# Kernel optimization log

Hardware: AMD Instinct MI355X
Metric: run time of the kernel (lower is better)

Reference implementation:

```python
import jax, jax.numpy as jnp
import numpy as np
from jax import lax

N, C_IN, HID, HP = 32, 512, 512, 28     # instances, channels, hidden, pooled res
NPATCH, HS = 25, 112                    # part channels (24+1), heatmap size
K_DYN, ATT_HID = 3, 64                  # dynamic-conv banks, attention hidden
BN_EPS = 1e-5


def setup_inputs() -> dict:
    key = jax.random.key(0)
    ks = jax.random.split(key, 20)
    g = lambda k, s, sc: sc * jax.random.normal(k, s, jnp.float32)

    features = g(ks[0], (N, C_IN, HP, HP), 1.0)
    # structured fine_segm so argmax class pattern covers all classes per row/col
    hh = jnp.arange(HS)[:, None]
    ww = jnp.arange(HS)[None, :]
    cls = (hh + ww) % NPATCH                                    # [H,W]
    base = 5.0 * jnp.transpose(jax.nn.one_hot(cls, NPATCH, dtype=jnp.float32), (2, 0, 1))
    fine_segm = base[None] + g(ks[1], (N, NPATCH, HS, HS), 0.5)
    u = jax.random.uniform(ks[2], (N, NPATCH, HS, HS), jnp.float32)
    v = jax.random.uniform(ks[3], (N, NPATCH, HS, HS), jnp.float32)

    return dict(
        features=features, fine_segm=fine_segm, u=u, v=v,
        conv1_w=g(ks[4], (HID, C_IN, 3, 3), 0.02), conv1_b=jnp.zeros((HID,), jnp.float32),
        conv2_w=g(ks[5], (HID, HID, 3, 3), 0.02), conv2_b=jnp.zeros((HID,), jnp.float32),
        att1_fc1_w=g(ks[6], (ATT_HID, 5), 0.1), att1_fc1_b=jnp.zeros((ATT_HID,), jnp.float32),
        att1_fc2_w=g(ks[7], (K_DYN, ATT_HID), 0.1), att1_fc2_b=jnp.zeros((K_DYN,), jnp.float32),
        dyn1_w=g(ks[8], (K_DYN, HID, HID, 3, 3), 0.02),
        att2_fc1_w=g(ks[9], (ATT_HID, 1), 0.1), att2_fc1_b=jnp.zeros((ATT_HID,), jnp.float32),
        att2_fc2_w=g(ks[10], (K_DYN, ATT_HID), 0.1), att2_fc2_b=jnp.zeros((K_DYN,), jnp.float32),
        dyn2_w=g(ks[11], (K_DYN, HID, HID, 3, 3), 0.02),
        bn1_g=1.0 + g(ks[12], (HID,), 0.1), bn1_b=g(ks[13], (HID,), 0.05),
        bn1_m=g(ks[14], (HID,), 0.1), bn1_v=jax.random.uniform(ks[15], (HID,), jnp.float32, 0.5, 1.5),
        bn2_g=1.0 + g(ks[16], (HID,), 0.1), bn2_b=g(ks[17], (HID,), 0.05),
        bn2_m=g(ks[18], (HID,), 0.1), bn2_v=jax.random.uniform(ks[19], (HID,), jnp.float32, 0.5, 1.5),
    )


def _conv2d(x, w, b=None):
    y = lax.conv_general_dilated(x, w, (1, 1), 'SAME',
                                 dimension_numbers=('NCHW', 'OIHW', 'NCHW'))
    return y if b is None else y + b[None, :, None, None]


def _bn(x, g, b, m, vv):
    inv = g / jnp.sqrt(vv + BN_EPS)
    return (x - m[None, :, None, None]) * inv[None, :, None, None] + b[None, :, None, None]


def _dyn_conv(stat, x, fc1_w, fc1_b, fc2_w, fc2_b, W):
    # attention over K kernel banks from globally pooled stats
    pooled = stat.mean(axis=(2, 3))                              # [B, Cin_att]
    h = jax.nn.relu(pooled @ fc1_w.T + fc1_b)                    # [B, ATT_HID]
    att = jax.nn.softmax(h @ fc2_w.T + fc2_b, axis=1)            # [B, K]
    Wb = jnp.einsum('bk,koihw->boihw', att, W)                   # per-sample kernels
    conv1 = lambda xi, wi: _conv2d(xi[None], wi)[0]
    return jax.vmap(conv1)(x, Wb)


def _local_linear(i, u, v):
    c = i.shape[1]
    mask = jnp.transpose(jax.nn.one_hot(jnp.argmax(i, axis=1), c, dtype=i.dtype), (0, 3, 1, 2))
    ue = (u * mask)[:, 1:]
    ve = (v * mask)[:, 1:]
    m = mask[:, 1:]
    u_mean = ue.sum(3, keepdims=True) / m.sum(3, keepdims=True)   # per-row mean
    v_mean = ve.sum(2, keepdims=True) / m.sum(2, keepdims=True)   # per-col mean
    u_var = jnp.sqrt((((ue - u_mean) ** 2) * m).sum(3) / m.sum(3))  # [B,C-1,H]
    v_var = jnp.sqrt((((ve - v_mean) ** 2) * m).sum(2) / m.sum(2))  # [B,C-1,W]
    var = jnp.sqrt(jnp.einsum('bch,bcw->bchw', u_var, v_var))
    return lax.stop_gradient(jnp.exp(-var.sum(1, keepdims=True)))   # [B,1,H,W]


def reference(features, fine_segm, u, v,
              conv1_w, conv1_b, conv2_w, conv2_b,
              att1_fc1_w, att1_fc1_b, att1_fc2_w, att1_fc2_b, dyn1_w,
              att2_fc1_w, att2_fc1_b, att2_fc2_w, att2_fc2_b, dyn2_w,
              bn1_g, bn1_b, bn1_m, bn1_v, bn2_g, bn2_b, bn2_m, bn2_v):
    x = jax.nn.relu(_conv2d(features, conv1_w, conv1_b))
    x = jax.nn.relu(_conv2d(x, conv2_w, conv2_b))
    identity = x

    p = jax.nn.softmax(fine_segm, axis=1)
    tv, _ = lax.top_k(jnp.moveaxis(p, 1, -1), 4)                 # [B,H,W,4]
    tv = jnp.moveaxis(tv, -1, 1)                                 # [B,4,H,W]
    stat1 = jnp.concatenate([tv, tv.mean(axis=1, keepdims=True)], axis=1)  # [B,5,H,W]
    stat2 = _local_linear(fine_segm, u, v)                       # [B,1,H,W]

    out = _dyn_conv(stat1, x, att1_fc1_w, att1_fc1_b, att1_fc2_w, att1_fc2_b, dyn1_w)
    out = jax.nn.relu(_bn(out, bn1_g, bn1_b, bn1_m, bn1_v))
    out = _dyn_conv(stat2, out, att2_fc1_w, att2_fc1_b, att2_fc2_w, att2_fc2_b, dyn2_w)
    out = _bn(out, bn2_g, bn2_b, bn2_m, bn2_v)
    return jax.nn.relu(out + identity)
```

## Files before the change

### kernel.cpp

```cpp
#include <hip/hip_runtime.h>
#include <math.h>

#define NB 32
#define CIN 512
#define HIDC 512
#define HP 28
#define PIX 784
#define NPCH 25
#define HS 112
#define HS2 12544
#define ATTH 64
#define BN_EPS 1e-5f

typedef unsigned short ushortT;
typedef __attribute__((ext_vector_type(8))) short s16x8;
typedef __attribute__((ext_vector_type(4))) float f32x4;

__device__ __forceinline__ float bf2f(unsigned bits16) {
    union { unsigned u; float f; } c; c.u = bits16 << 16; return c.f;
}
__device__ __forceinline__ unsigned f2bf_rne(float f) {
    union { float f; unsigned u; } c; c.f = f;
    unsigned u = c.u;
    u += 0x7FFFu + ((u >> 16) & 1u);
    return u >> 16;
}
__device__ __forceinline__ float asf_u(unsigned v) {
    union { unsigned u; float f; } c; c.u = v; return c.f;
}
__device__ __forceinline__ unsigned blendpair(unsigned u0, unsigned u1, unsigned u2,
                                              float a0, float a1, float a2) {
    float lo = a0*asf_u(u0 << 16) + a1*asf_u(u1 << 16) + a2*asf_u(u2 << 16);
    float hi = a0*asf_u(u0 & 0xFFFF0000u) + a1*asf_u(u1 & 0xFFFF0000u) + a2*asf_u(u2 & 0xFFFF0000u);
    union { float f; unsigned u; } cl, chh; cl.f = lo; chh.f = hi;
    return (cl.u >> 16) | (chh.u & 0xFFFF0000u);
}
__device__ __forceinline__ uint4 blend4(uint4 v0, uint4 v1, uint4 v2,
                                        float a0, float a1, float a2) {
    uint4 r;
    r.x = blendpair(v0.x, v1.x, v2.x, a0, a1, a2);
    r.y = blendpair(v0.y, v1.y, v2.y, a0, a1, a2);
    r.z = blendpair(v0.z, v1.z, v2.z, a0, a1, a2);
    r.w = blendpair(v0.w, v1.w, v2.w, a0, a1, a2);
    return r;
}

__global__ __launch_bounds__(256)
void nchw2nhwc_bf16(const float* __restrict__ in, ushortT* __restrict__ out)
{
    __shared__ float tile[64][65];
    const int b  = blockIdx.z;
    const int c0 = blockIdx.y * 64;
    const int p0 = blockIdx.x * 64;
    const int tid = threadIdx.x;
    for (int i = tid; i < 4096; i += 256) {
        int cc = i >> 6, pp = i & 63;
        float v = 0.f;
        if (p0 + pp < PIX) v = in[((size_t)b*CIN + c0 + cc)*PIX + p0 + pp];
        tile[cc][pp] = v;
    }
    __syncthreads();
    for (int i = tid; i < 4096; i += 256) {
        int pp = i >> 6, cc = i & 63;
        if (p0 + pp < PIX)
            out[((size_t)b*PIX + p0 + pp)*CIN + c0 + cc] = (ushortT)f2bf_rne(tile[cc][pp]);
    }
}

__global__ __launch_bounds__(256)
void wtrans_kernel(const float* __restrict__ w, ushortT* __restrict__ wt)
{
    __shared__ float buf[4608];
    const int oc = blockIdx.x, bank = blockIdx.y;
    const float* src = w + (size_t)bank*HIDC*CIN*9 + (size_t)oc*CIN*9;
    for (int i = threadIdx.x; i < 4608; i += 256) buf[i] = src[i];
    __syncthreads();
    for (int i = threadIdx.x; i < 4608; i += 256) {
        int t = i / 512, ic = i - t*512;
        wt[(((size_t)bank*9 + t)*HIDC + oc)*CIN + ic] = (ushortT)f2bf_rne(buf[(size_t)ic*9 + t]);
    }
}

template<int MODE>
__global__ __launch_bounds__(256, 2)
void conv_mfma(const ushortT* __restrict__ xin,
               const ushortT* __restrict__ wt,
               const float* __restrict__ bias,
               const float* __restrict__ scale,
               const float* __restrict__ shift,
               const float* __restrict__ att,
               const ushortT* __restrict__ addsrc,
               ushortT* __restrict__ outb,
               float* __restrict__ outf)
{
    __shared__ __align__(16) ushortT xs[480*64];
    __shared__ __align__(16) ushortT wsA[2][4096];

    const int tid  = threadIdx.x;
    const int lane = tid & 63;
    const int ph   = tid >> 6;
    const int lrow = lane & 15;
    const int lgrp = lane >> 4;

    const int oc0 = blockIdx.x * 64;
    const int sh  = blockIdx.y;
    const int b   = blockIdx.z;

    float a0 = 0.f, a1 = 0.f, a2 = 0.f;
    if (MODE != 0) { a0 = att[b*3+0]; a1 = att[b*3+1]; a2 = att[b*3+2]; }

    int pq[7];
#pragma unroll
    for (int nf = 0; nf < 7; ++nf) {
        int q = ph*98 + nf*16 + lrow;
        int qc = q < 392 ? q : 391;
        int r = qc / 28;
        pq[nf] = r*30 + (qc - r*28);
    }

    int afoff[2][4];
#pragma unroll
    for (int kk = 0; kk < 2; ++kk)
#pragma unroll
        for (int mf = 0; mf < 4; ++mf) {
            int ocl = mf*16 + lrow;
            afoff[kk][mf] = (ocl*8 + ((kk*4+lgrp) ^ (ocl&7)))*8;
        }

    int woff[2], wdst[2];
#pragma unroll
    for (int i = 0; i < 2; ++i) {
        int j = tid + i*256;
        int ocl = j >> 3, o = j & 7;
        woff[i] = ocl*CIN + o*8;
        wdst[i] = (ocl*8 + (o ^ (ocl&7)))*8;
    }

    f32x4 acc[4][7];
#pragma unroll
    for (int mf = 0; mf < 4; ++mf)
#pragma unroll
        for (int nf = 0; nf < 7; ++nf) acc[mf][nf] = (f32x4)0.f;

    const ushortT* xb = xin + (size_t)b * PIX * CIN;
    const size_t BANKS = (size_t)9*HIDC*CIN;

    auto stage_x = [&](int ic0) {
#pragma unroll
        for (int i = 0; i < 15; ++i) {
            int j = tid + i*256;
            int p = j >> 3, o = j & 7;
            int row = p / 30, col = p - row*30;
            int gh = sh*14 + row - 1, gw = col - 1;
            uint4 val = make_uint4(0u,0u,0u,0u);
            if ((unsigned)gh < 28u && (unsigned)gw < 28u)
                val = *(const uint4*)(xb + ((size_t)(gh*28 + gw)*CIN + ic0 + o*8));
            *(uint4*)(xs + (size_t)((p*8 + (o ^ (p&7)))*8)) = val;
        }
    };

    stage_x(0);
    {
        const ushortT* wA = wt + (size_t)oc0*CIN;
#pragma unroll
        for (int i = 0; i < 2; ++i) {
            uint4 v0 = *(const uint4*)(wA + woff[i]);
            uint4 val = v0;
            if (MODE != 0) {
                uint4 v1 = *(const uint4*)(wA + woff[i] + BANKS);
                uint4 v2 = *(const uint4*)(wA + woff[i] + 2*BANKS);
                val = blend4(v0, v1, v2, a0, a1, a2);
            }
            *(uint4*)(&wsA[0][0] + wdst[i]) = val;
        }
    }
    __syncthreads();

    uint4 p0[2], p1[2], p2[2];
    for (int k = 0; k < 72; ++k) {
        const int ch  = k / 9;
        const int t   = k - ch*9;
        const int cur = k & 1;
        const bool pf = (k < 71);
        const int kn  = k + 1;
        const int chn = kn / 9, tn = kn - chn*9;

        if (pf) {
            const ushortT* wA = wt + ((size_t)tn*HIDC + oc0)*CIN + chn*64;
#pragma unroll
            for (int i = 0; i < 2; ++i) {
                p0[i] = *(const uint4*)(wA + woff[i]);
                if (MODE != 0) {
                    p1[i] = *(const uint4*)(wA + woff[i] + BANKS);
                    p2[i] = *(const uint4*)(wA + woff[i] + 2*BANKS);
                }
            }
        }

        const int dh = (t >= 6) ? 2 : (t >= 3 ? 1 : 0);
        const int dw = t - dh*3;
        const int doff = dh*30 + dw;
        const ushortT* wbuf = &wsA[cur][0];
#pragma unroll
        for (int kk = 0; kk < 2; ++kk) {
            const int ob = kk*4 + lgrp;
            s16x8 af[4];
#pragma unroll
            for (int mf = 0; mf < 4; ++mf)
                af[mf] = *(const s16x8*)(wbuf + afoff[kk][mf]);
#pragma unroll
            for (int nf = 0; nf < 7; ++nf) {
                int pp = pq[nf] + doff;
                s16x8 bv = *(const s16x8*)(xs + (size_t)((pp*8 + (ob ^ (pp&7)))*8));
#pragma unroll
                for (int mf = 0; mf < 4; ++mf)
                    acc[mf][nf] = __builtin_amdgcn_mfma_f32_16x16x32_bf16(af[mf], bv, acc[mf][nf], 0, 0, 0);
            }
        }

        if (pf) {
            ushortT* wb = &wsA[cur^1][0];
#pragma unroll
            for (int i = 0; i < 2; ++i) {
                uint4 val;
                if (MODE == 0) val = p0[i];
                else           val = blend4(p0[i], p1[i], p2[i], a0, a1, a2);
                *(uint4*)(wb + wdst[i]) = val;
            }
            if (t == 8) {
                __syncthreads();
                stage_x(chn*64);
            }
        }
        __syncthreads();
    }

    const int q0 = ph * 98;
#pragma unroll
    for (int mf = 0; mf < 4; ++mf) {
        const int oc = oc0 + mf*16 + lgrp*4;
        float sc[4], shv[4];
#pragma unroll
        for (int jj = 0; jj < 4; ++jj) {
            if (MODE == 0) { sc[jj] = 1.f; shv[jj] = bias[oc+jj]; }
            else           { sc[jj] = scale[oc+jj]; shv[jj] = shift[oc+jj]; }
        }
#pragma unroll
        for (int nf = 0; nf < 7; ++nf) {
            const int qrel = nf*16 + lrow;
            if (qrel < 98) {
                const int p = sh*392 + q0 + qrel;
                f32x4 a = acc[mf][nf];
                if (MODE == 2) {
                    const ushortT* id = addsrc + ((size_t)b*PIX + p)*CIN + oc;
                    ushort4 iv = *(const ushort4*)id;
                    float v0 = fmaxf(a.x*sc[0] + shv[0] + bf2f(iv.x), 0.f);
                    float v1 = fmaxf(a.y*sc[1] + shv[1] + bf2f(iv.y), 0.f);
                    float v2 = fmaxf(a.z*sc[2] + shv[2] + bf2f(iv.z), 0.f);
                    float v3 = fmaxf(a.w*sc[3] + shv[3] + bf2f(iv.w), 0.f);
                    float* op = outf + ((size_t)b*HIDC + oc)*PIX + p;
                    op[0*PIX] = v0; op[1*PIX] = v1; op[2*PIX] = v2; op[3*PIX] = v3;
                } else {
                    float v0 = fmaxf(a.x*sc[0] + shv[0], 0.f);
                    float v1 = fmaxf(a.y*sc[1] + shv[1], 0.f);
                    float v2 = fmaxf(a.z*sc[2] + shv[2], 0.f);
                    float v3 = fmaxf(a.w*sc[3] + shv[3], 0.f);
                    ushort4 o4;
                    o4.x = (ushortT)f2bf_rne(v0); o4.y = (ushortT)f2bf_rne(v1);
                    o4.z = (ushortT)f2bf_rne(v2); o4.w = (ushortT)f2bf_rne(v3);
                    *(ushort4*)(outb + ((size_t)b*PIX + p)*CIN + oc) = o4;
                }
            }
        }
    }
}

template<int MODE>
__global__ __launch_bounds__(256)
void conv3x3_kernel(const float* __restrict__ x,
                    const float* __restrict__ w,
                    const float* __restrict__ bias,
                    const float* __restrict__ att,
                    const float* __restrict__ bnscale,
                    const float* __restrict__ bnshift,
                    const float* __restrict__ addsrc,
                    float* __restrict__ out)
{
    const int tid = threadIdx.x;
    const int o0  = blockIdx.x * 8;
    const int b   = blockIdx.y;
    __shared__ float xsb[30*30];
    __shared__ float wsm[72];
    float a0 = 0.f, a1 = 0.f, a2 = 0.f;
    if (MODE != 0) { a0 = att[b*3+0]; a1 = att[b*3+1]; a2 = att[b*3+2]; }
    float acc[8][4];
#pragma unroll
    for (int o = 0; o < 8; ++o)
#pragma unroll
        for (int s = 0; s < 4; ++s) acc[o][s] = 0.f;
    const float* xbp = x + (size_t)b * CIN * PIX;
    for (int i = 0; i < CIN; ++i) {
        const float* xc = xbp + (size_t)i * PIX;
        for (int idx = tid; idx < 900; idx += 256) {
            int r = idx / 30, c = idx - r*30;
            float v = 0.f;
            if (r >= 1 && r <= HP && c >= 1 && c <= HP) v = xc[(r-1)*HP + (c-1)];
            xsb[idx] = v;
        }
        if (tid < 72) {
            int o = tid / 9, tap = tid - o*9;
            float wv;
            if (MODE == 0) wv = w[((size_t)(o0+o)*CIN + i)*9 + tap];
            else {
                size_t base = ((size_t)(o0+o)*CIN + i)*9 + tap;
                size_t bank = (size_t)HIDC*CIN*9;
                wv = a0*w[base] + a1*w[base+bank] + a2*w[base+2*bank];
            }
            wsm[tid] = wv;
        }
        __syncthreads();
        float xwin[4][9];
#pragma unroll
        for (int s = 0; s < 4; ++s) {
            int p = tid + s*256; if (p > PIX-1) p = PIX-1;
            int h = p / HP, wc = p - h*HP;
#pragma unroll
            for (int t = 0; t < 9; ++t) {
                int dh = t/3, dw = t - dh*3;
                xwin[s][t] = xsb[(h+dh)*30 + (wc+dw)];
            }
        }
#pragma unroll
        for (int o = 0; o < 8; ++o) {
            float wr[9];
#pragma unroll
            for (int t = 0; t < 9; ++t) wr[t] = wsm[o*9+t];
#pragma unroll
            for (int s = 0; s < 4; ++s) {
                float sum = acc[o][s];
#pragma unroll
                for (int t = 0; t < 9; ++t) sum = fmaf(wr[t], xwin[s][t], sum);
                acc[o][s] = sum;
            }
        }
        __syncthreads();
    }
#pragma unroll
    for (int s = 0; s < 4; ++s) {
        int p = tid + s*256;
        if (p >= PIX) continue;
#pragma unroll
        for (int o = 0; o < 8; ++o) {
            int oc = o0 + o;
            float v = acc[o][s];
            if (MODE == 0) v += bias[oc];
            else           v = v * bnscale[oc] + bnshift[oc];
            if (MODE == 2) v += addsrc[((size_t)b*HIDC + oc)*PIX + p];
            v = fmaxf(v, 0.f);
            out[((size_t)b*HIDC + oc)*PIX + p] = v;
        }
    }
}

__global__ __launch_bounds__(256)
void stat1_kernel(const float* __restrict__ fs, float* __restrict__ part)
{
    const int b = blockIdx.y, chunk = blockIdx.x, tid = threadIdx.x;
    const float* f = fs + (size_t)b * NPCH * HS2;
    const int lo = chunk * 14 * HS, hi = lo + 14 * HS;
    float s0=0.f, s1=0.f, s2=0.f, s3=0.f;
    for (int pos = lo + tid; pos < hi; pos += 256) {
        float t0=-1e30f, t1=-1e30f, t2=-1e30f, t3=-1e30f;
        for (int c = 0; c < NPCH; ++c) {
            float v = f[(size_t)c*HS2 + pos];
            if      (v > t0) { t3=t2; t2=t1; t1=t0; t0=v; }
            else if (v > t1) { t3=t2; t2=t1; t1=v; }
            else if (v > t2) { t3=t2; t2=v; }
            else if (v > t3) { t3=v; }
        }
        float denom = 0.f;
        for (int c = 0; c < NPCH; ++c) denom += expf(f[(size_t)c*HS2 + pos] - t0);
        float inv = 1.f / denom;
        s0 += inv;
        s1 += expf(t1 - t0) * inv;
        s2 += expf(t2 - t0) * inv;
        s3 += expf(t3 - t0) * inv;
    }
    __shared__ float red[256];
    float vals[4] = {s0, s1, s2, s3};
    for (int j = 0; j < 4; ++j) {
        red[tid] = vals[j];
        __syncthreads();
        for (int off = 128; off; off >>= 1) {
            if (tid < off) red[tid] += red[tid + off];
            __syncthreads();
        }
        if (tid == 0) part[((size_t)b*8 + chunk)*4 + j] = red[0];
        __syncthreads();
    }
}

__global__ void cls_kernel(const float* __restrict__ fs, int* __restrict__ cls)
{
    int idx = blockIdx.x*256 + threadIdx.x;
    if (idx >= NB*HS2) return;
    int b = idx / HS2, pos = idx - b*HS2;
    const float* f = fs + (size_t)b*NPCH*HS2 + pos;
    float best = f[0]; int bi = 0;
    for (int c = 1; c < NPCH; ++c) {
        float v = f[(size_t)c*HS2];
        if (v > best) { best = v; bi = c; }
    }
    cls[idx] = bi;
}

__global__ __launch_bounds__(256)
void rowstat_kernel(const float* __restrict__ u, const int* __restrict__ cls,
                    float* __restrict__ uvar)
{
    int wid = blockIdx.x*4 + (threadIdx.x >> 6);
    int lane = threadIdx.x & 63;
    int h = wid % HS, t = wid / HS, c = t % 24, b = t / 24;
    const int*   cr = cls + (size_t)b*HS2 + (size_t)h*HS;
    const float* ur = u + (((size_t)b*NPCH + c + 1)*HS + h)*HS;
    float cnt = 0.f, s = 0.f, s2 = 0.f;
    for (int wc = lane; wc < HS; wc += 64) {
        if (cr[wc] == c + 1) { float v = ur[wc]; cnt += 1.f; s += v; s2 += v*v; }
    }
    for (int off = 32; off; off >>= 1) {
        cnt += __shfl_down(cnt, off);
        s   += __shfl_down(s, off);
        s2  += __shfl_down(s2, off);
    }
    if (lane == 0) {
        float mean = s / cnt;
        uvar[wid] = sqrtf(fmaxf(s2/cnt - mean*mean, 0.f));
    }
}

__global__ void colstat_kernel(const float* __restrict__ v, const int* __restrict__ cls,
                               float* __restrict__ vvar)
{
    int idx = blockIdx.x*256 + threadIdx.x;
    if (idx >= NB*24*HS) return;
    int wc = idx % HS, t = idx / HS, c = t % 24, b = t / 24;
    const int*   cbase = cls + (size_t)b*HS2 + wc;
    const float* vbase = v + (((size_t)b*NPCH + c + 1)*HS)*HS + wc;
    float cnt = 0.f, s = 0.f, s2 = 0.f;
    for (int h = 0; h < HS; ++h) {
        if (cbase[(size_t)h*HS] == c + 1) {
            float val = vbase[(size_t)h*HS];
            cnt += 1.f; s += val; s2 += val*val;
        }
    }
    float mean = s / cnt;
    vvar[idx] = sqrtf(fmaxf(s2/cnt - mean*mean, 0.f));
}

__global__ __launch_bounds__(256)
void stat2_kernel(const float* __restrict__ uvar, const float* __restrict__ vvar,
                  float* __restrict__ pooled2p)
{
    const int b = blockIdx.x, seg = blockIdx.y, tid = threadIdx.x;
    __shared__ float us[24*HS], vs[24*HS], red[256];
    for (int i = tid; i < 24*HS; i += 256) {
        us[i] = uvar[(size_t)b*24*HS + i];
        vs[i] = vvar[(size_t)b*24*HS + i];
    }
    __syncthreads();
    float local = 0.f;
    const int lo = seg*1568, hi = lo + 1568;
    for (int pos = lo + tid; pos < hi; pos += 256) {
        int h = pos / HS, wc = pos - h*HS;
        float sum = 0.f;
        for (int c = 0; c < 24; ++c) sum += sqrtf(us[c*HS+h] * vs[c*HS+wc]);
        local += expf(-sum);
    }
    red[tid] = local;
    __syncthreads();
    for (int off = 128; off; off >>= 1) {
        if (tid < off) red[tid] += red[tid + off];
        __syncthreads();
    }
    if (tid == 0) pooled2p[b*8 + seg] = red[0];
}

__global__ __launch_bounds__(256)
void mlp_kernel(const float* __restrict__ part, const float* __restrict__ pooled2p,
                const float* __restrict__ a1w1, const float* __restrict__ a1b1,
                const float* __restrict__ a1w2, const float* __restrict__ a1b2,
                const float* __restrict__ a2w1, const float* __restrict__ a2b1,
                const float* __restrict__ a2w2, const float* __restrict__ a2b2,
                const float* __restrict__ bn1g, const float* __restrict__ bn1b,
                const float* __restrict__ bn1m, const float* __restrict__ bn1v,
                const float* __restrict__ bn2g, const float* __restrict__ bn2b,
                const float* __restrict__ bn2m, const float* __restrict__ bn2v,
                float* __restrict__ att1, float* __restrict__ att2,
                float* __restrict__ bnsc)
{
    const int tid = threadIdx.x;
    if (tid < NB) {
        int b = tid;
        float p[5]; float tot = 0.f;
        for (int j = 0; j < 4; ++j) {
            float s = 0.f;
            for (int ch = 0; ch < 8; ++ch) s += part[((size_t)b*8 + ch)*4 + j];
            p[j] = s / (float)HS2; tot += p[j];
        }
        p[4] = tot * 0.25f;
        float lg[3] = {a1b2[0], a1b2[1], a1b2[2]};
        for (int j = 0; j < ATTH; ++j) {
            float hv = a1b1[j];
            for (int t = 0; t < 5; ++t) hv += a1w1[j*5+t] * p[t];
            hv = fmaxf(hv, 0.f);
            for (int k = 0; k < 3; ++k) lg[k] += a1w2[k*ATTH+j] * hv;
        }
        float mx = fmaxf(fmaxf(lg[0], lg[1]), lg[2]);
        float e0 = expf(lg[0]-mx), e1 = expf(lg[1]-mx), e2 = expf(lg[2]-mx);
        float inv = 1.f / (e0+e1+e2);
        att1[b*3+0] = e0*inv; att1[b*3+1] = e1*inv; att1[b*3+2] = e2*inv;
    } else if (tid < 2*NB) {
        int b = tid - NB;
        float psum = 0.f;
        for (int j = 0; j < 8; ++j) psum += pooled2p[b*8 + j];
        float p = psum / (float)HS2;
        float lg[3] = {a2b2[0], a2b2[1], a2b2[2]};
        for (int j = 0; j < ATTH; ++j) {
            float hv = fmaxf(a2b1[j] + a2w1[j] * p, 0.f);
            for (int k = 0; k < 3; ++k) lg[k] += a2w2[k*ATTH+j] * hv;
        }
        float mx = fmaxf(fmaxf(lg[0], lg[1]), lg[2]);
        float e0 = expf(lg[0]-mx), e1 = expf(lg[1]-mx), e2 = expf(lg[2]-mx);
        float inv = 1.f / (e0+e1+e2);
        att2[b*3+0] = e0*inv; att2[b*3+1] = e1*inv; att2[b*3+2] = e2*inv;
    }
    for (int o = tid; o < HIDC; o += 256) {
        float sc1 = bn1g[o] / sqrtf(bn1v[o] + BN_EPS);
        bnsc[o]          = sc1;
        bnsc[512 + o]    = bn1b[o] - bn1m[o]*sc1;
        float sc2 = bn2g[o] / sqrtf(bn2v[o] + BN_EPS);
        bnsc[1024 + o]   = sc2;
        bnsc[1536 + o]   = bn2b[o] - bn2m[o]*sc2;
    }
}

extern "C" void kernel_launch(void* const* d_in, const int* in_sizes, int n_in,
                              void* d_out, int out_size, void* d_ws, size_t ws_size,
                              hipStream_t stream)
{
    (void)in_sizes; (void)n_in; (void)out_size;
    const float* features = (const float*)d_in[0];
    const float* fine_segm= (const float*)d_in[1];
    const float* u        = (const float*)d_in[2];
    const float* v        = (const float*)d_in[3];
    const float* conv1_w  = (const float*)d_in[4];
    const float* conv1_b  = (const float*)d_in[5];
    const float* conv2_w  = (const float*)d_in[6];
    const float* conv2_b  = (const float*)d_in[7];
    const float* a1w1     = (const float*)d_in[8];
    const float* a1b1     = (const float*)d_in[9];
    const float* a1w2     = (const float*)d_in[10];
    const float* a1b2     = (const float*)d_in[11];
    const float* dyn1_w   = (const float*)d_in[12];
    const float* a2w1     = (const float*)d_in[13];
    const float* a2b1     = (const float*)d_in[14];
    const float* a2w2     = (const float*)d_in[15];
    const float* a2b2     = (const float*)d_in[16];
    const float* dyn2_w   = (const float*)d_in[17];
    const float* bn1g     = (const float*)d_in[18];
    const float* bn1b     = (const float*)d_in[19];
    const float* bn1m     = (const float*)d_in[20];
    const float* bn1v     = (const float*)d_in[21];
    const float* bn2g     = (const float*)d_in[22];
    const float* bn2b     = (const float*)d_in[23];
    const float* bn2m     = (const float*)d_in[24];
    const float* bn2v     = (const float*)d_in[25];

    const size_t XB_BYTES = (size_t)NB*PIX*CIN*2;
    const size_t WT_BYTES = (size_t)3*9*HIDC*CIN*2;
    const size_t NEED = XB_BYTES*2 + WT_BYTES + 2308096;

    if (ws_size >= NEED) {
        char* wsb = (char*)d_ws;
        ushortT* xbuf = (ushortT*)wsb;
        ushortT* x2   = (ushortT*)(wsb + XB_BYTES);
        ushortT* wt   = (ushortT*)(wsb + 2*XB_BYTES);
        float* sm     = (float*)(wsb + 2*XB_BYTES + WT_BYTES);
        float* part    = sm;  sm += 1024;
        float* pooled2 = sm;  sm += 256;
        float* att1    = sm;  sm += 96;
        float* att2    = sm;  sm += 96;
        float* bnsc    = sm;  sm += 2048;
        float* uvar    = sm;  sm += NB*24*HS;
        float* vvar    = sm;  sm += NB*24*HS;
        int*   cls     = (int*)sm;
        ushortT* x1    = (ushortT*)d_out;

        nchw2nhwc_bf16<<<dim3(13, 8, NB), 256, 0, stream>>>(features, xbuf);
        wtrans_kernel<<<dim3(512, 1), 256, 0, stream>>>(conv1_w, wt);
        conv_mfma<0><<<dim3(8, 2, NB), 256, 0, stream>>>(
            xbuf, wt, conv1_b, nullptr, nullptr, nullptr, nullptr, x1, nullptr);
        wtrans_kernel<<<dim3(512, 1), 256, 0, stream>>>(conv2_w, wt);
        conv_mfma<0><<<dim3(8, 2, NB), 256, 0, stream>>>(
            x1, wt, conv2_b, nullptr, nullptr, nullptr, nullptr, x2, nullptr);

        stat1_kernel<<<dim3(8, NB), 256, 0, stream>>>(fine_segm, part);
        cls_kernel<<<(NB*HS2 + 255)/256, 256, 0, stream>>>(fine_segm, cls);
        rowstat_kernel<<<(NB*24*HS)/4, 256, 0, stream>>>(u, cls, uvar);
        colstat_kernel<<<(NB*24*HS + 255)/256, 256, 0, stream>>>(v, cls, vvar);
        stat2_kernel<<<dim3(NB, 8), 256, 0, stream>>>(uvar, vvar, pooled2);
        mlp_kernel<<<1, 256, 0, stream>>>(part, pooled2,
            a1w1, a1b1, a1w2, a1b2, a2w1, a2b1, a2w2, a2b2,
            bn1g, bn1b, bn1m, bn1v, bn2g, bn2b, bn2m, bn2v,
            att1, att2, bnsc);

        wtrans_kernel<<<dim3(512, 3), 256, 0, stream>>>(dyn1_w, wt);
        conv_mfma<1><<<dim3(8, 2, NB), 256, 0, stream>>>(
            x2, wt, nullptr, bnsc, bnsc + 512, att1, nullptr, xbuf, nullptr);
        wtrans_kernel<<<dim3(512, 3), 256, 0, stream>>>(dyn2_w, wt);
        conv_mfma<2><<<dim3(8, 2, NB), 256, 0, stream>>>(
            xbuf, wt, nullptr, bnsc + 1024, bnsc + 1536, att2, x2, nullptr, (float*)d_out);
    } else {
        const size_t BIG = (size_t)NB * HIDC * PIX;
        float* x1y1 = (float*)d_out;
        float* ws0  = (float*)d_ws;
        float* sm   = ws0 + BIG;
        float* part    = sm;  sm += 1024;
        float* pooled2 = sm;  sm += 256;
        float* att1    = sm;  sm += 96;
        float* att2    = sm;  sm += 96;
        float* bnsc    = sm;  sm += 2048;
        float* uvar    = sm;  sm += NB*24*HS;
        float* vvar    = sm;  sm += NB*24*HS;
        int*   cls     = (int*)sm;

        conv3x3_kernel<0><<<dim3(64, NB), 256, 0, stream>>>(
            features, conv1_w, conv1_b, nullptr, nullptr, nullptr, nullptr, x1y1);
        conv3x3_kernel<0><<<dim3(64, NB), 256, 0, stream>>>(
            x1y1, conv2_w, conv2_b, nullptr, nullptr, nullptr, nullptr, ws0);
        stat1_kernel<<<dim3(8, NB), 256, 0, stream>>>(fine_segm, part);
        cls_kernel<<<(NB*HS2 + 255)/256, 256, 0, stream>>>(fine_segm, cls);
        rowstat_kernel<<<(NB*24*HS)/4, 256, 0, stream>>>(u, cls, uvar);
        colstat_kernel<<<(NB*24*HS + 255)/256, 256, 0, stream>>>(v, cls, vvar);
        stat2_kernel<<<dim3(NB, 8), 256, 0, stream>>>(uvar, vvar, pooled2);
        mlp_kernel<<<1, 256, 0, stream>>>(part, pooled2,
            a1w1, a1b1, a1w2, a1b2, a2w1, a2b1, a2w2, a2b2,
            bn1g, bn1b, bn1m, bn1v, bn2g, bn2b, bn2m, bn2v,
            att1, att2, bnsc);
        conv3x3_kernel<1><<<dim3(64, NB), 256, 0, stream>>>(
            ws0, dyn1_w, nullptr, att1, bnsc, bnsc + 512, nullptr, x1y1);
        conv3x3_kernel<2><<<dim3(64, NB), 256, 0, stream>>>(
            x1y1, dyn2_w, nullptr, att2, bnsc + 1024, bnsc + 1536, ws0, ws0);
        hipMemcpyAsync(d_out, ws0, BIG * sizeof(float), hipMemcpyDeviceToDevice, stream);
    }
}
```

Before: 825.5 us.

## Software-pipeline LDS B-fragment loads in conv MFMA loop and fuse argmax into stat1

Restructures the conv MFMA inner loop into channel-chunk by tap loops with double-buffered register B fragments (PB/QB). Next tap's B loads are issued while the current half's MFMAs run, and MFMA blocks are wrapped in s_setprio. The intent is to hide LDS read latency behind matrix work, at the cost of more VGPR use. Separately, the argmax class computation is folded into the stat1 top-4 kernel, removing one kernel launch and a second full read of fine_segm.

```diff
diff --git a/kernel.cpp b/kernel.cpp
--- a/kernel.cpp
+++ b/kernel.cpp
@@ -158,6 +158,9 @@
             *(uint4*)(xs + (size_t)((p*8 + (o ^ (p&7)))*8)) = val;
         }
     };
+    auto baddr = [&](int pp) {
+        return (pp*8 + (lgrp ^ (pp&7)))*16;
+    };
 
     stage_x(0);
     {
@@ -176,63 +179,88 @@
     }
     __syncthreads();
 
+    s16x8 PB[7], QB[7];
     uint4 p0[2], p1[2], p2[2];
-    for (int k = 0; k < 72; ++k) {
-        const int ch  = k / 9;
-        const int t   = k - ch*9;
-        const int cur = k & 1;
-        const bool pf = (k < 71);
-        const int kn  = k + 1;
-        const int chn = kn / 9, tn = kn - chn*9;
-
-        if (pf) {
-            const ushortT* wA = wt + ((size_t)tn*HIDC + oc0)*CIN + chn*64;
-#pragma unroll
-            for (int i = 0; i < 2; ++i) {
-                p0[i] = *(const uint4*)(wA + woff[i]);
-                if (MODE != 0) {
-                    p1[i] = *(const uint4*)(wA + woff[i] + BANKS);
-                    p2[i] = *(const uint4*)(wA + woff[i] + 2*BANKS);
+
+    for (int c = 0; c < 8; ++c) {
+#pragma unroll
+        for (int nf = 0; nf < 7; ++nf)
+            PB[nf] = *(const s16x8*)((const char*)xs + baddr(pq[nf]));
+
+#pragma unroll
+        for (int t = 0; t < 9; ++t) {
+            const int k   = c*9 + t;
+            const int cur = k & 1;
+            const bool pf = (k < 71);
+            const int tn  = (t == 8) ? 0 : (t + 1);
+            const int chn = (t == 8) ? (c + 1) : c;
+            const ushortT* wbuf = &wsA[cur][0];
+
+            if (pf) {
+                const ushortT* wA = wt + ((size_t)tn*HIDC + oc0)*CIN + chn*64;
+#pragma unroll
+                for (int i = 0; i < 2; ++i) {
+                    p0[i] = *(const uint4*)(wA + woff[i]);
+                    if (MODE != 0) {
+                        p1[i] = *(const uint4*)(wA + woff[i] + BANKS);
+                        p2[i] = *(const uint4*)(wA + woff[i] + 2*BANKS);
+                    }
                 }
             }
-        }
-
-        const int dh = (t >= 6) ? 2 : (t >= 3 ? 1 : 0);
-        const int dw = t - dh*3;
-        const int doff = dh*30 + dw;
-        const ushortT* wbuf = &wsA[cur][0];
-#pragma unroll
-        for (int kk = 0; kk < 2; ++kk) {
-            const int ob = kk*4 + lgrp;
-            s16x8 af[4];
+
+            const int doff  = (t/3)*30 + (t%3);
+            const int doffn = ((t+1)/3)*30 + ((t+1)%3);
+
+            s16x8 af0[4];
 #pragma unroll
             for (int mf = 0; mf < 4; ++mf)
-                af[mf] = *(const s16x8*)(wbuf + afoff[kk][mf]);
-#pragma unroll
-            for (int nf = 0; nf < 7; ++nf) {
-                int pp = pq[nf] + doff;
-                s16x8 bv = *(const s16x8*)(xs + (size_t)((pp*8 + (ob ^ (pp&7)))*8));
+                af0[mf] = *(const s16x8*)(wbuf + afoff[0][mf]);
+#pragma unroll
+            for (int nf = 0; nf < 7; ++nf)
+                QB[nf] = *(const s16x8*)((const char*)xs + (baddr(pq[nf]+doff) ^ 64));
+
+            __builtin_amdgcn_s_setprio(1);
+#pragma unroll
+            for (int nf = 0; nf < 7; ++nf)
 #pragma unroll
                 for (int mf = 0; mf < 4; ++mf)
-                    acc[mf][nf] = __builtin_amdgcn_mfma_f32_16x16x32_bf16(af[mf], bv, acc[mf][nf], 0, 0, 0);
-            }
-        }
-
-        if (pf) {
-            ushortT* wb = &wsA[cur^1][0];
-#pragma unroll
-            for (int i = 0; i < 2; ++i) {
-                uint4 val;
-                if (MODE == 0) val = p0[i];
-                else           val = blend4(p0[i], p1[i], p2[i], a0, a1, a2);
-                *(uint4*)(wb + wdst[i]) = val;
-            }
-            if (t == 8) {
-                __syncthreads();
-                stage_x(chn*64);
-            }
-        }
-        __syncthreads();
+                    acc[mf][nf] = __builtin_amdgcn_mfma_f32_16x16x32_bf16(af0[mf], PB[nf], acc[mf][nf], 0, 0, 0);
+            __builtin_amdgcn_s_setprio(0);
+
+            s16x8 af1[4];
+#pragma unroll
+            for (int mf = 0; mf < 4; ++mf)
+                af1[mf] = *(const s16x8*)(wbuf + afoff[1][mf]);
+            if (t < 8) {
+#pragma unroll
+                for (int nf = 0; nf < 7; ++nf)
+                    PB[nf] = *(const s16x8*)((const char*)xs + baddr(pq[nf]+doffn));
+            }
+
+            __builtin_amdgcn_s_setprio(1);
+#pragma unroll
+            for (int nf = 0; nf < 7; ++nf)
+#pragma unroll
+                for (int mf = 0; mf < 4; ++mf)
+                    acc[mf][nf] = __builtin_amdgcn_mfma_f32_16x16x32_bf16(af1[mf], QB[nf], acc[mf][nf], 0, 0, 0);
+            __builtin_amdgcn_s_setprio(0);
+
+            if (pf) {
+                ushortT* wb = &wsA[cur^1][0];
+#pragma unroll
+                for (int i = 0; i < 2; ++i) {
+                    uint4 val;
+                    if (MODE == 0) val = p0[i];
+                    else           val = blend4(p0[i], p1[i], p2[i], a0, a1, a2);
+                    *(uint4*)(wb + wdst[i]) = val;
+                }
+                if (t == 8) {
+                    __syncthreads();
+                    stage_x(chn*64);
+                }
+            }
+            __syncthreads();
+        }
     }
 
     const int q0 = ph * 98;
@@ -363,7 +391,8 @@
 }
 
 __global__ __launch_bounds__(256)
-void stat1_kernel(const float* __restrict__ fs, float* __restrict__ part)
+void stat1cls_kernel(const float* __restrict__ fs, float* __restrict__ part,
+                     int* __restrict__ cls)
 {
     const int b = blockIdx.y, chunk = blockIdx.x, tid = threadIdx.x;
     const float* f = fs + (size_t)b * NPCH * HS2;
@@ -371,13 +400,15 @@
     float s0=0.f, s1=0.f, s2=0.f, s3=0.f;
     for (int pos = lo + tid; pos < hi; pos += 256) {
         float t0=-1e30f, t1=-1e30f, t2=-1e30f, t3=-1e30f;
+        int bi = 0;
         for (int c = 0; c < NPCH; ++c) {
             float v = f[(size_t)c*HS2 + pos];
-            if      (v > t0) { t3=t2; t2=t1; t1=t0; t0=v; }
+            if      (v > t0) { t3=t2; t2=t1; t1=t0; t0=v; bi=c; }
             else if (v > t1) { t3=t2; t2=t1; t1=v; }
             else if (v > t2) { t3=t2; t2=v; }
             else if (v > t3) { t3=v; }
         }
+        cls[(size_t)b*HS2 + pos] = bi;
         float denom = 0.f;
         for (int c = 0; c < NPCH; ++c) denom += expf(f[(size_t)c*HS2 + pos] - t0);
         float inv = 1.f / denom;
@@ -398,20 +429,6 @@
         if (tid == 0) part[((size_t)b*8 + chunk)*4 + j] = red[0];
         __syncthreads();
     }
-}
-
-__global__ void cls_kernel(const float* __restrict__ fs, int* __restrict__ cls)
-{
-    int idx = blockIdx.x*256 + threadIdx.x;
-    if (idx >= NB*HS2) return;
-    int b = idx / HS2, pos = idx - b*HS2;
-    const float* f = fs + (size_t)b*NPCH*HS2 + pos;
-    float best = f[0]; int bi = 0;
-    for (int c = 1; c < NPCH; ++c) {
-        float v = f[(size_t)c*HS2];
-        if (v > best) { best = v; bi = c; }
-    }
-    cls[idx] = bi;
 }
 
 __global__ __launch_bounds__(256)
@@ -604,8 +621,7 @@
         conv_mfma<0><<<dim3(8, 2, NB), 256, 0, stream>>>(
             x1, wt, conv2_b, nullptr, nullptr, nullptr, nullptr, x2, nullptr);
 
-        stat1_kernel<<<dim3(8, NB), 256, 0, stream>>>(fine_segm, part);
-        cls_kernel<<<(NB*HS2 + 255)/256, 256, 0, stream>>>(fine_segm, cls);
+        stat1cls_kernel<<<dim3(8, NB), 256, 0, stream>>>(fine_segm, part, cls);
         rowstat_kernel<<<(NB*24*HS)/4, 256, 0, stream>>>(u, cls, uvar);
         colstat_kernel<<<(NB*24*HS + 255)/256, 256, 0, stream>>>(v, cls, vvar);
         stat2_kernel<<<dim3(NB, 8), 256, 0, stream>>>(uvar, vvar, pooled2);
@@ -638,8 +654,7 @@
             features, conv1_w, conv1_b, nullptr, nullptr, nullptr, nullptr, x1y1);
         conv3x3_kernel<0><<<dim3(64, NB), 256, 0, stream>>>(
             x1y1, conv2_w, conv2_b, nullptr, nullptr, nullptr, nullptr, ws0);
-        stat1_kernel<<<dim3(8, NB), 256, 0, stream>>>(fine_segm, part);
-        cls_kernel<<<(NB*HS2 + 255)/256, 256, 0, stream>>>(fine_segm, cls);
+        stat1cls_kernel<<<dim3(8, NB), 256, 0, stream>>>(fine_segm, part, cls);
         rowstat_kernel<<<(NB*24*HS)/4, 256, 0, stream>>>(u, cls, uvar);
         colstat_kernel<<<(NB*24*HS + 255)/256, 256, 0, stream>>>(v, cls, vvar);
         stat2_kernel<<<dim3(NB, 8), 256, 0, stream>>>(uvar, vvar, pooled2);
```

After: 1.472 ms. 1.78x slower.
